# Kernel optimization log

Measured on AMD Instinct MI355X. Metric: run time of the kernel, lower is better.

Reference implementation:

```python
import jax, jax.numpy as jnp
import numpy as np

EPS = 1e-10

def _iou(a, b):
    """IoU for boxes in (cx, cy, w, h) format; a, b: (..., 4)."""
    a_min = a[..., :2] - a[..., 2:] * 0.5
    a_max = a[..., :2] + a[..., 2:] * 0.5
    b_min = b[..., :2] - b[..., 2:] * 0.5
    b_max = b[..., :2] + b[..., 2:] * 0.5
    inter_wh = jnp.clip(jnp.minimum(a_max, b_max) - jnp.maximum(a_min, b_min), 0.0)
    inter = inter_wh[..., 0] * inter_wh[..., 1]
    area_a = a[..., 2] * a[..., 3]
    area_b = b[..., 2] * b[..., 3]
    return inter / (area_a + area_b - inter + EPS)

def setup_inputs() -> dict:
    key = jax.random.key(0)
    k1, k2, k3 = jax.random.split(key, 3)
    BATCH, S, C = 16384, 7, 30
    # uniform in (0.01, 1) so sqrt() of w,h channels is finite/differentiable
    preds = jax.random.uniform(k1, (BATCH, S, S, C), jnp.float32, 0.01, 1.0)
    labels = jax.random.uniform(k2, (BATCH, S, S, C), jnp.float32, 0.01, 1.0)
    obj = jax.random.bernoulli(k3, 0.15, (BATCH, S, S)).astype(jnp.float32)
    labels = labels.at[..., 4].set(obj)  # code branches on labels[...,4] == 1
    return {"preds": preds, "labels": labels}

def reference(preds, labels):
    batch = preds.shape[0]
    obj = labels[..., 4] == 1.0  # (B, S, S)
    # faithful quirk: label bbox x-coord is read transposed (labels[i, y, x, 0])
    lb0 = jnp.swapaxes(labels[..., 0], 1, 2)
    lbox = jnp.stack([lb0, labels[..., 1], labels[..., 2], labels[..., 3]], axis=-1)
    iou1 = _iou(preds[..., 0:4], lbox)
    iou2 = _iou(preds[..., 5:9], lbox)
    choose1 = iou1 > iou2
    # branch where box 1 is responsible
    b1 = (5.0 * jnp.sum((preds[..., 0:2] - labels[..., 0:2]) ** 2, -1)
          + jnp.sum((jnp.sqrt(preds[..., 2:4]) - jnp.sqrt(labels[..., 2:4])) ** 2, -1)
          + (iou1 - preds[..., 4]) ** 2
          + 0.5 * preds[..., 9] ** 2)
    # branch where box 2 is responsible (targets read from labels[...,5:9] as in source)
    b2 = (5.0 * jnp.sum((preds[..., 5:7] - labels[..., 5:7]) ** 2, -1)
          + jnp.sum((jnp.sqrt(preds[..., 7:9]) - jnp.sqrt(labels[..., 7:9])) ** 2, -1)
          + (iou2 - preds[..., 9]) ** 2
          + 0.5 * preds[..., 4] ** 2)
    cls = jnp.sum((labels[..., 10:] - preds[..., 10:]) ** 2, -1)
    obj_loss = jnp.where(choose1, b1, b2) + cls
    noobj_loss = 0.5 * (preds[..., 4] ** 2 + preds[..., 9] ** 2)
    total = jnp.sum(jnp.where(obj, obj_loss, noobj_loss))
    return total / batch
```

## Files before the change

kernel.cpp:

```cpp
#include <hip/hip_runtime.h>


#define BATCH 16384
#define S 7
#define C 30
#define NCELLS (BATCH * S * S)
#define BLOCK 64
#define TILES 4
#define CELLS_PER_TILE 64
#define CELLS_PER_BLOCK (TILES * CELLS_PER_TILE)
#define NBLK (NCELLS / CELLS_PER_BLOCK)

#define SL_OFF   0
#define TAILP_OFF 1920
#define SP_OFF   2048
#define LDS_FLOATS 3968

#define GLOBAL_LOAD_LDS16(g, l)                                         \
    __builtin_amdgcn_global_load_lds(                                   \
        (const __attribute__((address_space(1))) void*)(g),             \
        (__attribute__((address_space(3))) void*)(l), 16, 0, 0)

__device__ __forceinline__ float sq(float v) { return v * v; }

__device__ __forceinline__ float iou_box(float acx, float acy, float aw, float ah,
                                         float bcx, float bcy, float bw, float bh) {
    float ax0 = acx - aw * 0.5f, ax1 = acx + aw * 0.5f;
    float ay0 = acy - ah * 0.5f, ay1 = acy + ah * 0.5f;
    float bx0 = bcx - bw * 0.5f, bx1 = bcx + bw * 0.5f;
    float by0 = bcy - bh * 0.5f, by1 = bcy + bh * 0.5f;
    float iw = fmaxf(fminf(ax1, bx1) - fmaxf(ax0, bx0), 0.0f);
    float ih = fmaxf(fminf(ay1, by1) - fmaxf(ay0, by0), 0.0f);
    float inter = iw * ih;
    float denom = aw * ah + bw * bh - inter + 1e-10f;
    return inter / denom;
}

__global__ __launch_bounds__(BLOCK) void yolo_partial_kernel(
        const float* __restrict__ preds,
        const float* __restrict__ labels,
        float* __restrict__ partials) {
    __shared__ __align__(16) float lds[LDS_FLOATS];

    const int tid = threadIdx.x;
    float tsum[TILES];

    #pragma unroll
    for (int t = 0; t < TILES; ++t) {
        const int base_cell = blockIdx.x * CELLS_PER_BLOCK + t * CELLS_PER_TILE;
        const float4* gp = reinterpret_cast<const float4*>(preds  + (size_t)base_cell * C);
        const float4* gl = reinterpret_cast<const float4*>(labels + (size_t)base_cell * C);

        __syncthreads();

        #pragma unroll
        for (int k = 0; k < 7; ++k)
            GLOBAL_LOAD_LDS16(gl + k * 64 + tid, (char*)lds + (size_t)k * 1024);
        #pragma unroll
        for (int k = 0; k < 7; ++k)
            GLOBAL_LOAD_LDS16(gp + k * 64 + tid,
                              (char*)lds + (size_t)SP_OFF * 4 + (size_t)k * 1024);
        {
            const float4* src = (tid < 32) ? (gl + 448 + tid) : (gp + 448 + (tid - 32));
            GLOBAL_LOAD_LDS16(src, (char*)lds + 7168);
        }

        const int cell = base_cell + tid;
        const int b    = cell / (S * S);
        const int rem  = cell - b * (S * S);
        const int y    = rem / S;
        const int x    = rem - y * S;
        const int pc   = b * (S * S) + x * S + y;
        const float lb0 = labels[(size_t)pc * C];

        __syncthreads();

        {
            float2 v = *reinterpret_cast<const float2*>(&lds[TAILP_OFF + 2 * tid]);
            *reinterpret_cast<float2*>(&lds[SP_OFF + 1792 + 2 * tid]) = v;
        }
        __syncthreads();

        const float* p = &lds[SP_OFF + tid * C];
        const float* l = &lds[SL_OFF + tid * C];
        float pv[C], lv[C];
        #pragma unroll
        for (int i = 0; i < C / 2; ++i) {
            float2 tp = *reinterpret_cast<const float2*>(p + 2 * i);
            pv[2 * i] = tp.x; pv[2 * i + 1] = tp.y;
            float2 tl = *reinterpret_cast<const float2*>(l + 2 * i);
            lv[2 * i] = tl.x; lv[2 * i + 1] = tl.y;
        }

        float iou1 = iou_box(pv[0], pv[1], pv[2], pv[3], lb0, lv[1], lv[2], lv[3]);
        float iou2 = iou_box(pv[5], pv[6], pv[7], pv[8], lb0, lv[1], lv[2], lv[3]);

        float b1 = 5.0f * (sq(pv[0] - lv[0]) + sq(pv[1] - lv[1]))
                 + sq(sqrtf(pv[2]) - sqrtf(lv[2])) + sq(sqrtf(pv[3]) - sqrtf(lv[3]))
                 + sq(iou1 - pv[4])
                 + 0.5f * pv[9] * pv[9];

        float b2 = 5.0f * (sq(pv[5] - lv[5]) + sq(pv[6] - lv[6]))
                 + sq(sqrtf(pv[7]) - sqrtf(lv[7])) + sq(sqrtf(pv[8]) - sqrtf(lv[8]))
                 + sq(iou2 - pv[9])
                 + 0.5f * pv[4] * pv[4];

        float cls = 0.0f;
        #pragma unroll
        for (int c = 10; c < C; ++c) cls += sq(lv[c] - pv[c]);

        float obj_loss   = ((iou1 > iou2) ? b1 : b2) + cls;
        float noobj_loss = 0.5f * (pv[4] * pv[4] + pv[9] * pv[9]);
        float loss = (lv[4] == 1.0f) ? obj_loss : noobj_loss;

        #pragma unroll
        for (int off = 32; off > 0; off >>= 1)
            loss += __shfl_down(loss, off, 64);
        tsum[t] = loss;
    }

    if (tid == 0) {
        partials[blockIdx.x] = ((tsum[0] + tsum[1]) + tsum[2]) + tsum[3];
    }
}

__global__ __launch_bounds__(256) void yolo_reduce_kernel(
        const float* __restrict__ partials,
        float* __restrict__ out) {
    const int tid = threadIdx.x;
    float s = 0.0f;
    for (int i = tid; i < NBLK; i += 256) s += partials[i];

    #pragma unroll
    for (int off = 32; off > 0; off >>= 1)
        s += __shfl_down(s, off, 64);

    __shared__ float wsum[4];
    int lane = tid & 63;
    int wv   = tid >> 6;
    if (lane == 0) wsum[wv] = s;
    __syncthreads();
    if (tid == 0) {
        out[0] = (wsum[0] + wsum[1] + wsum[2] + wsum[3]) * (1.0f / (float)BATCH);
    }
}

extern "C" void kernel_launch(void* const* d_in, const int* in_sizes, int n_in,
                              void* d_out, int out_size, void* d_ws, size_t ws_size,
                              hipStream_t stream) {
    const float* preds  = (const float*)d_in[0];
    const float* labels = (const float*)d_in[1];
    float* out = (float*)d_out;
    float* partials = (float*)d_ws;

    yolo_partial_kernel<<<NBLK, BLOCK, 0, stream>>>(preds, labels, partials);
    yolo_reduce_kernel<<<1, 256, 0, stream>>>(partials, out);
}
```

Baseline: 214.4 us.

## Split per-block tiles across four waves with private LDS regions

Previously each block was a single 64-thread wave that worked through four tiles of 64 cells one after another, with block barriers between the loads and the compute. Now each block has four waves, and each wave loads and computes its own tile in its own slice of LDS at the same time as the others. Each wave waits only on its own memory counter instead of a block barrier, and the four wave sums are combined through shared memory. The cost is about 63 KB of LDS per block, which limits how many blocks fit on a CU and may leave the number of loads in flight per CU roughly unchanged.

```diff
diff --git a/kernel.cpp b/kernel.cpp
--- a/kernel.cpp
+++ b/kernel.cpp
@@ -5,16 +5,12 @@
 #define S 7
 #define C 30
 #define NCELLS (BATCH * S * S)
-#define BLOCK 64
-#define TILES 4
-#define CELLS_PER_TILE 64
-#define CELLS_PER_BLOCK (TILES * CELLS_PER_TILE)
+#define BLOCK 256
+#define CELLS_PER_BLOCK 256
 #define NBLK (NCELLS / CELLS_PER_BLOCK)
 
-#define SL_OFF   0
-#define TAILP_OFF 1920
-#define SP_OFF   2048
-#define LDS_FLOATS 3968
+#define SP_BASE 8192
+#define LDS_FLOATS (8192 + 4 * 1920)
 
 #define GLOBAL_LOAD_LDS16(g, l)                                         \
     __builtin_amdgcn_global_load_lds(                                   \
@@ -41,86 +37,85 @@
         const float* __restrict__ labels,
         float* __restrict__ partials) {
     __shared__ __align__(16) float lds[LDS_FLOATS];
+    __shared__ float wsum[4];
 
-    const int tid = threadIdx.x;
-    float tsum[TILES];
+    const int tid  = threadIdx.x;
+    const int lane = tid & 63;
+    const int wv   = tid >> 6;
+    const int cell0 = blockIdx.x * CELLS_PER_BLOCK + wv * 64;
+
+    const float4* gp = reinterpret_cast<const float4*>(preds  + (size_t)cell0 * C);
+    const float4* gl = reinterpret_cast<const float4*>(labels + (size_t)cell0 * C);
+    float* sl = &lds[wv * 2048];
+    float* sp = &lds[SP_BASE + wv * 1920];
 
     #pragma unroll
-    for (int t = 0; t < TILES; ++t) {
-        const int base_cell = blockIdx.x * CELLS_PER_BLOCK + t * CELLS_PER_TILE;
-        const float4* gp = reinterpret_cast<const float4*>(preds  + (size_t)base_cell * C);
-        const float4* gl = reinterpret_cast<const float4*>(labels + (size_t)base_cell * C);
-
-        __syncthreads();
-
-        #pragma unroll
-        for (int k = 0; k < 7; ++k)
-            GLOBAL_LOAD_LDS16(gl + k * 64 + tid, (char*)lds + (size_t)k * 1024);
-        #pragma unroll
-        for (int k = 0; k < 7; ++k)
-            GLOBAL_LOAD_LDS16(gp + k * 64 + tid,
-                              (char*)lds + (size_t)SP_OFF * 4 + (size_t)k * 1024);
-        {
-            const float4* src = (tid < 32) ? (gl + 448 + tid) : (gp + 448 + (tid - 32));
-            GLOBAL_LOAD_LDS16(src, (char*)lds + 7168);
-        }
-
-        const int cell = base_cell + tid;
-        const int b    = cell / (S * S);
-        const int rem  = cell - b * (S * S);
-        const int y    = rem / S;
-        const int x    = rem - y * S;
-        const int pc   = b * (S * S) + x * S + y;
-        const float lb0 = labels[(size_t)pc * C];
-
-        __syncthreads();
-
-        {
-            float2 v = *reinterpret_cast<const float2*>(&lds[TAILP_OFF + 2 * tid]);
-            *reinterpret_cast<float2*>(&lds[SP_OFF + 1792 + 2 * tid]) = v;
-        }
-        __syncthreads();
-
-        const float* p = &lds[SP_OFF + tid * C];
-        const float* l = &lds[SL_OFF + tid * C];
-        float pv[C], lv[C];
-        #pragma unroll
-        for (int i = 0; i < C / 2; ++i) {
-            float2 tp = *reinterpret_cast<const float2*>(p + 2 * i);
-            pv[2 * i] = tp.x; pv[2 * i + 1] = tp.y;
-            float2 tl = *reinterpret_cast<const float2*>(l + 2 * i);
-            lv[2 * i] = tl.x; lv[2 * i + 1] = tl.y;
-        }
-
-        float iou1 = iou_box(pv[0], pv[1], pv[2], pv[3], lb0, lv[1], lv[2], lv[3]);
-        float iou2 = iou_box(pv[5], pv[6], pv[7], pv[8], lb0, lv[1], lv[2], lv[3]);
-
-        float b1 = 5.0f * (sq(pv[0] - lv[0]) + sq(pv[1] - lv[1]))
-                 + sq(sqrtf(pv[2]) - sqrtf(lv[2])) + sq(sqrtf(pv[3]) - sqrtf(lv[3]))
-                 + sq(iou1 - pv[4])
-                 + 0.5f * pv[9] * pv[9];
-
-        float b2 = 5.0f * (sq(pv[5] - lv[5]) + sq(pv[6] - lv[6]))
-                 + sq(sqrtf(pv[7]) - sqrtf(lv[7])) + sq(sqrtf(pv[8]) - sqrtf(lv[8]))
-                 + sq(iou2 - pv[9])
-                 + 0.5f * pv[4] * pv[4];
-
-        float cls = 0.0f;
-        #pragma unroll
-        for (int c = 10; c < C; ++c) cls += sq(lv[c] - pv[c]);
-
-        float obj_loss   = ((iou1 > iou2) ? b1 : b2) + cls;
-        float noobj_loss = 0.5f * (pv[4] * pv[4] + pv[9] * pv[9]);
-        float loss = (lv[4] == 1.0f) ? obj_loss : noobj_loss;
-
-        #pragma unroll
-        for (int off = 32; off > 0; off >>= 1)
-            loss += __shfl_down(loss, off, 64);
-        tsum[t] = loss;
+    for (int k = 0; k < 7; ++k)
+        GLOBAL_LOAD_LDS16(gl + k * 64 + lane, (char*)sl + (size_t)k * 1024);
+    #pragma unroll
+    for (int k = 0; k < 7; ++k)
+        GLOBAL_LOAD_LDS16(gp + k * 64 + lane, (char*)sp + (size_t)k * 1024);
+    {
+        const float4* src = (lane < 32) ? (gl + 448 + lane) : (gp + 448 + (lane - 32));
+        GLOBAL_LOAD_LDS16(src, (char*)sl + 7168);
     }
 
+    const int cell = cell0 + lane;
+    const int b    = cell / (S * S);
+    const int rem  = cell - b * (S * S);
+    const int y    = rem / S;
+    const int x    = rem - y * S;
+    const int pc   = b * (S * S) + x * S + y;
+    const float lb0 = labels[(size_t)pc * C];
+
+    asm volatile("s_waitcnt vmcnt(0)" ::: "memory");
+    __builtin_amdgcn_sched_barrier(0);
+
+    {
+        float2 v = *reinterpret_cast<const float2*>(&sl[1920 + 2 * lane]);
+        *reinterpret_cast<float2*>(&sp[1792 + 2 * lane]) = v;
+    }
+
+    const float* p = sp + lane * C;
+    const float* l = sl + lane * C;
+    float pv[C], lv[C];
+    #pragma unroll
+    for (int i = 0; i < C / 2; ++i) {
+        float2 tp = *reinterpret_cast<const float2*>(p + 2 * i);
+        pv[2 * i] = tp.x; pv[2 * i + 1] = tp.y;
+        float2 tl = *reinterpret_cast<const float2*>(l + 2 * i);
+        lv[2 * i] = tl.x; lv[2 * i + 1] = tl.y;
+    }
+
+    float iou1 = iou_box(pv[0], pv[1], pv[2], pv[3], lb0, lv[1], lv[2], lv[3]);
+    float iou2 = iou_box(pv[5], pv[6], pv[7], pv[8], lb0, lv[1], lv[2], lv[3]);
+
+    float b1 = 5.0f * (sq(pv[0] - lv[0]) + sq(pv[1] - lv[1]))
+             + sq(sqrtf(pv[2]) - sqrtf(lv[2])) + sq(sqrtf(pv[3]) - sqrtf(lv[3]))
+             + sq(iou1 - pv[4])
+             + 0.5f * pv[9] * pv[9];
+
+    float b2 = 5.0f * (sq(pv[5] - lv[5]) + sq(pv[6] - lv[6]))
+             + sq(sqrtf(pv[7]) - sqrtf(lv[7])) + sq(sqrtf(pv[8]) - sqrtf(lv[8]))
+             + sq(iou2 - pv[9])
+             + 0.5f * pv[4] * pv[4];
+
+    float cls = 0.0f;
+    #pragma unroll
+    for (int c = 10; c < C; ++c) cls += sq(lv[c] - pv[c]);
+
+    float obj_loss   = ((iou1 > iou2) ? b1 : b2) + cls;
+    float noobj_loss = 0.5f * (pv[4] * pv[4] + pv[9] * pv[9]);
+    float loss = (lv[4] == 1.0f) ? obj_loss : noobj_loss;
+
+    #pragma unroll
+    for (int off = 32; off > 0; off >>= 1)
+        loss += __shfl_down(loss, off, 64);
+
+    if (lane == 0) wsum[wv] = loss;
+    __syncthreads();
     if (tid == 0) {
-        partials[blockIdx.x] = ((tsum[0] + tsum[1]) + tsum[2]) + tsum[3];
+        partials[blockIdx.x] = wsum[0] + wsum[1] + wsum[2] + wsum[3];
     }
 }
 
```

Measured after the change: 205.4 us. 4.2% less time.
